# Optimization experiments

Hardware: AMD Instinct MI355X
Metric: run time of the kernel (lower is better)

Reference implementation:

```python
import jax, jax.numpy as jnp
import numpy as np

B, S, D, H, DFF = 4, 2048, 1024, 16, 4096
DK = D // H


def layer_norm(x, g, b, eps=1e-5):
    mu = jnp.mean(x, axis=-1, keepdims=True)
    var = jnp.mean((x - mu) ** 2, axis=-1, keepdims=True)
    return (x - mu) / jnp.sqrt(var + eps) * g + b


def setup_inputs() -> dict:
    key = jax.random.key(0)
    ks = jax.random.split(key, 16)
    w = lambda k, shape: jax.random.normal(k, shape, jnp.float32) * 0.02
    return {
        "x": jax.random.normal(ks[0], (B, S, D), jnp.float32),
        "w_q": w(ks[1], (D, D)), "b_q": jnp.zeros((D,), jnp.float32),
        "w_k": w(ks[2], (D, D)), "b_k": jnp.zeros((D,), jnp.float32),
        "w_v": w(ks[3], (D, D)), "b_v": jnp.zeros((D,), jnp.float32),
        "w_o": w(ks[4], (D, D)), "b_o": jnp.zeros((D,), jnp.float32),
        "w_g": w(ks[5], (D, H)), "b_g": jnp.zeros((H,), jnp.float32),
        "w1": w(ks[6], (D, DFF)), "b1": jnp.zeros((DFF,), jnp.float32),
        "w2": w(ks[7], (DFF, D)), "b2": jnp.zeros((D,), jnp.float32),
        "g1": jnp.ones((D,), jnp.float32), "beta1": jnp.zeros((D,), jnp.float32),
        "g2": jnp.ones((D,), jnp.float32), "beta2": jnp.zeros((D,), jnp.float32),
        "mask": jnp.ones((B, 1, 1, S), jnp.int32),
    }


def reference(x, w_q, b_q, w_k, b_k, w_v, b_v, w_o, b_o, w_g, b_g,
              w1, b1, w2, b2, g1, beta1, g2, beta2, mask):
    b, s, d = x.shape
    scale = DK ** -0.5
    # QKV projections -> [B,H,S,DK]
    q = (x @ w_q + b_q).reshape(b, s, H, DK).transpose(0, 2, 1, 3)
    k = (x @ w_k + b_k).reshape(b, s, H, DK).transpose(0, 2, 1, 3)
    v = (x @ w_v + b_v).reshape(b, s, H, DK).transpose(0, 2, 1, 3)
    scores = jnp.einsum("bhqd,bhkd->bhqk", q, k) * scale  # [B,H,S,S]
    scores = jnp.where(mask == 0, jnp.float32(-1e9), scores)
    attn = jax.nn.softmax(scores, axis=-1)
    # per-(token, head) sigmoid gate applied post-softmax
    gate = jax.nn.sigmoid(x @ w_g + b_g)            # [B,S,H]
    attn = attn * gate.transpose(0, 2, 1)[..., None]  # [B,H,S,1]
    ctx = jnp.einsum("bhqk,bhkd->bhqd", attn, v)
    ctx = ctx.transpose(0, 2, 1, 3).reshape(b, s, d)
    attn_out = ctx @ w_o + b_o
    x1 = layer_norm(x + attn_out, g1, beta1)
    ff = jax.nn.gelu(x1 @ w1 + b1, approximate=False) @ w2 + b2
    return layer_norm(x1 + ff, g2, beta2)
```

## Files before the change

### kernel.cpp

```cpp
#include <hip/hip_runtime.h>
#include <hip/hip_bf16.h>
#include <cstdint>


typedef __bf16 bf16x8 __attribute__((ext_vector_type(8)));
typedef float  f32x4  __attribute__((ext_vector_type(4)));

__device__ __forceinline__ uint16_t f2bf_bits(float f) {
    __hip_bfloat16 h = __float2bfloat16(f);
    return __builtin_bit_cast(uint16_t, h);
}

#define GLOAD16(ldsb, gp) __builtin_amdgcn_global_load_lds( \
    (const __attribute__((address_space(1))) void*)(gp),    \
    (__attribute__((address_space(3))) void*)(ldsb), 16, 0, 0)

__global__ __launch_bounds__(256) void cast_bf16_kernel(
    const float* __restrict__ in, __hip_bfloat16* __restrict__ out, size_t n4)
{
    size_t i = (size_t)blockIdx.x * blockDim.x + threadIdx.x;
    if (i >= n4) return;
    float4 v = ((const float4*)in)[i];
    ushort4 o;
    o.x = f2bf_bits(v.x); o.y = f2bf_bits(v.y);
    o.z = f2bf_bits(v.z); o.w = f2bf_bits(v.w);
    ((ushort4*)out)[i] = o;
}

__global__ __launch_bounds__(256) void transpose_cast_kernel(
    const float* __restrict__ in, __hip_bfloat16* __restrict__ out, int K, int N)
{
    __shared__ float t[32][33];
    int n0 = blockIdx.x * 32, k0 = blockIdx.y * 32;
    int tx = threadIdx.x, ty = threadIdx.y;
#pragma unroll
    for (int i = 0; i < 4; ++i)
        t[ty + i * 8][tx] = in[(size_t)(k0 + ty + i * 8) * N + n0 + tx];
    __syncthreads();
#pragma unroll
    for (int i = 0; i < 4; ++i)
        out[(size_t)(n0 + ty + i * 8) * K + k0 + tx] = __float2bfloat16(t[tx][ty + i * 8]);
}

__global__ __launch_bounds__(256) void gate_kernel(
    const float* __restrict__ x, const float* __restrict__ wg,
    const float* __restrict__ bg, float* __restrict__ gate)
{
    int tid = threadIdx.x, lane = tid & 63, wid = tid >> 6;
    int row = blockIdx.x * 4 + wid;
    const float* xr = x + (size_t)row * 1024;
    float acc[16];
#pragma unroll
    for (int hh = 0; hh < 16; ++hh) acc[hh] = 0.0f;
    for (int k = lane; k < 1024; k += 64) {
        float xv = xr[k];
        const float* wr = wg + (size_t)k * 16;
#pragma unroll
        for (int hh = 0; hh < 16; ++hh) acc[hh] = fmaf(xv, wr[hh], acc[hh]);
    }
#pragma unroll
    for (int hh = 0; hh < 16; ++hh) {
#pragma unroll
        for (int d = 1; d < 64; d <<= 1) acc[hh] += __shfl_xor(acc[hh], d);
    }
    if (lane < 16) {
        float v = 0.0f;
#pragma unroll
        for (int hh = 0; hh < 16; ++hh)
            if (lane == hh) v = acc[hh] + bg[hh];
        gate[(size_t)row * 16 + lane] = 1.0f / (1.0f + __expf(-v));
    }
}

__global__ __launch_bounds__(256) void ln_kernel(
    const float* __restrict__ A, const float* __restrict__ Bx,
    const float* __restrict__ g, const float* __restrict__ beta,
    float* __restrict__ outf, __hip_bfloat16* __restrict__ outb)
{
    int row = blockIdx.x, tid = threadIdx.x;
    const float4* a4 = (const float4*)(A  + (size_t)row * 1024);
    const float4* b4 = (const float4*)(Bx + (size_t)row * 1024);
    float4 va = a4[tid], vb = b4[tid];
    float x0 = va.x + vb.x, x1 = va.y + vb.y, x2 = va.z + vb.z, x3 = va.w + vb.w;
    float s  = x0 + x1 + x2 + x3;
    float sq = x0 * x0 + x1 * x1 + x2 * x2 + x3 * x3;
#pragma unroll
    for (int d = 1; d < 64; d <<= 1) { s += __shfl_xor(s, d); sq += __shfl_xor(sq, d); }
    __shared__ float ss[4], ssq[4];
    int wid = tid >> 6, lane = tid & 63;
    if (lane == 0) { ss[wid] = s; ssq[wid] = sq; }
    __syncthreads();
    s  = ss[0] + ss[1] + ss[2] + ss[3];
    sq = ssq[0] + ssq[1] + ssq[2] + ssq[3];
    float mean = s * (1.0f / 1024.0f);
    float var  = sq * (1.0f / 1024.0f) - mean * mean;
    float rstd = rsqrtf(var + 1e-5f);
    float4 gv = ((const float4*)g)[tid], bv = ((const float4*)beta)[tid];
    float y0 = (x0 - mean) * rstd * gv.x + bv.x;
    float y1 = (x1 - mean) * rstd * gv.y + bv.y;
    float y2 = (x2 - mean) * rstd * gv.z + bv.z;
    float y3 = (x3 - mean) * rstd * gv.w + bv.w;
    float4 o; o.x = y0; o.y = y1; o.z = y2; o.w = y3;
    ((float4*)(outf + (size_t)row * 1024))[tid] = o;
    if (outb) {
        ushort4 ob;
        ob.x = f2bf_bits(y0); ob.y = f2bf_bits(y1);
        ob.z = f2bf_bits(y2); ob.w = f2bf_bits(y3);
        ((ushort4*)(outb + (size_t)row * 1024))[tid] = ob;
    }
}

template<int EPI>
__global__ __launch_bounds__(256, 2) void gemm128(
    const __hip_bfloat16* __restrict__ A,
    const __hip_bfloat16* __restrict__ BT,
    const float* __restrict__ bias,
    void* __restrict__ Cout, int M, int N, int K)
{
    __shared__ __align__(16) __hip_bfloat16 As[128 * 64];
    __shared__ __align__(16) __hip_bfloat16 Bs[128 * 64];
    const int tid = threadIdx.x, lane = tid & 63, wid = tid >> 6;
    const int bx = blockIdx.x, by = blockIdx.y;
    const int wr = wid >> 1, wc = wid & 1;

    f32x4 acc[4][4];
#pragma unroll
    for (int i = 0; i < 4; ++i)
#pragma unroll
        for (int j = 0; j < 4; ++j) acc[i][j] = (f32x4){0.f, 0.f, 0.f, 0.f};

    const char* Abase = (const char*)A  + (size_t)(by * 128) * K * 2;
    const char* Bbase = (const char*)BT + (size_t)(bx * 128) * K * 2;
    char* AsB = (char*)As; char* BsB = (char*)Bs;
    const int laneRow = lane >> 3;
    const int laneCol = (lane & 7) * 16;

    for (int ks = 0; ks < K; ks += 64) {
#pragma unroll
        for (int j = 0; j < 4; ++j) {
            int r = j * 32 + wid * 8 + laneRow;
            size_t goff = (size_t)r * K * 2 + (size_t)ks * 2 + laneCol;
            GLOAD16(AsB + j * 4096 + wid * 1024, Abase + goff);
            GLOAD16(BsB + j * 4096 + wid * 1024, Bbase + goff);
        }
        __syncthreads();
#pragma unroll
        for (int kk = 0; kk < 2; ++kk) {
            const int kob = (kk * 32 + (lane >> 4) * 8) * 2;
            bf16x8 a[4], b[4];
#pragma unroll
            for (int mt = 0; mt < 4; ++mt)
                a[mt] = *(const bf16x8*)(AsB + (wr * 64 + mt * 16 + (lane & 15)) * 128 + kob);
#pragma unroll
            for (int nt = 0; nt < 4; ++nt)
                b[nt] = *(const bf16x8*)(BsB + (wc * 64 + nt * 16 + (lane & 15)) * 128 + kob);
#pragma unroll
            for (int mt = 0; mt < 4; ++mt)
#pragma unroll
                for (int nt = 0; nt < 4; ++nt)
                    acc[mt][nt] = __builtin_amdgcn_mfma_f32_16x16x32_bf16(
                        a[mt], b[nt], acc[mt][nt], 0, 0, 0);
        }
        __syncthreads();
    }

    const int m0 = by * 128 + wr * 64;
    const int n0 = bx * 128 + wc * 64;
#pragma unroll
    for (int mt = 0; mt < 4; ++mt) {
#pragma unroll
        for (int nt = 0; nt < 4; ++nt) {
            int n = n0 + nt * 16 + (lane & 15);
            float bv = bias[n];
#pragma unroll
            for (int j = 0; j < 4; ++j) {
                int m = m0 + mt * 16 + (lane >> 4) * 4 + j;
                float v = acc[mt][nt][j] + bv;
                ((float*)Cout)[(size_t)m * N + n] = v;
            }
        }
    }
}

template<int EPI>
__global__ __launch_bounds__(512, 2) void gemm256(
    const __hip_bfloat16* __restrict__ A,
    const __hip_bfloat16* __restrict__ BT,
    const float* __restrict__ bias0,
    const float* __restrict__ bias1,
    const float* __restrict__ bias2,
    __hip_bfloat16* __restrict__ out0,
    __hip_bfloat16* __restrict__ out1,
    __hip_bfloat16* __restrict__ out2,
    int M, int N, int K)
{
    __shared__ __align__(16) char lds_[131072];
    const int tid = threadIdx.x;
    const int lane = tid & 63;
    const int l15 = lane & 15;
    const int wid = tid >> 6;
    const int wm = wid >> 2, wn = wid & 3;

    const int NBX = N >> 8;
    const int cpx = ((M >> 8) * NBX) >> 3;
    const int nl = ((int)blockIdx.x & 7) * cpx + ((int)blockIdx.x >> 3);
    const int by = nl / NBX, bx = nl % NBX;

    const char* Abase = (const char*)A  + (size_t)(by * 256) * K * 2;
    const char* Bbase = (const char*)BT + (size_t)(bx * 256) * K * 2;

    const int srow = tid >> 3;
    const int ssw  = ((tid & 7) ^ (srow & 7)) * 16;

    f32x4 acc[8][4];
#pragma unroll
    for (int i = 0; i < 8; ++i)
#pragma unroll
        for (int j = 0; j < 4; ++j) acc[i][j] = (f32x4){0.f, 0.f, 0.f, 0.f};

    auto stageA = [&](int d, int c, int ks) {
        const char* src = Abase + ((size_t)(c * 64 + srow) * K + ks) * 2 + ssw;
        GLOAD16(lds_ + d * 65536 + c * 8192 + wid * 1024, src);
    };
    auto stageB = [&](int d, int c, int ks) {
        const char* src = Bbase + ((size_t)(c * 64 + srow) * K + ks) * 2 + ssw;
        GLOAD16(lds_ + d * 65536 + 32768 + c * 8192 + wid * 1024, src);
    };

    const int NT = K >> 6;
    stageB(0, 0, 0); stageB(0, 1, 0); stageB(0, 2, 0); stageB(0, 3, 0);
    stageA(0, 0, 0); stageA(0, 2, 0); stageA(0, 1, 0); stageA(0, 3, 0);
    asm volatile("s_waitcnt vmcnt(0)" ::: "memory");
    __builtin_amdgcn_s_barrier();

    for (int t = 0; t < NT; ++t) {
        const int cur = t & 1, nxt = cur ^ 1;
        const int ksn = (t + 1) << 6;
        const bool st = (t + 1 < NT);
        const char* ldsA = lds_ + cur * 65536;
        const char* ldsB = ldsA + 32768;

        bf16x8 bfr[4][2];
#pragma unroll
        for (int p = 0; p < 4; ++p) {
            if (p == 0) {
#pragma unroll
                for (int nf = 0; nf < 4; ++nf) {
                    const int br = wn * 64 + nf * 16 + l15;
#pragma unroll
                    for (int kk = 0; kk < 2; ++kk) {
                        const int kb = kk * 64 + (lane >> 4) * 16;
                        bfr[nf][kk] = *(const bf16x8*)(ldsB + (br >> 6) * 8192 +
                            (br & 63) * 128 + (kb ^ ((br & 7) << 4)));
                    }
                }
            }
            bf16x8 afr[2][2];
#pragma unroll
            for (int mi = 0; mi < 2; ++mi) {
                const int ar = wm * 128 + (2 * p + mi) * 16 + l15;
#pragma unroll
                for (int kk = 0; kk < 2; ++kk) {
                    const int kb = kk * 64 + (lane >> 4) * 16;
                    afr[mi][kk] = *(const bf16x8*)(ldsA + (ar >> 6) * 8192 +
                        (ar & 63) * 128 + (kb ^ ((ar & 7) << 4)));
                }
            }
            if (st) {
                if      (p == 0) { stageB(nxt, 0, ksn); stageB(nxt, 1, ksn); }
                else if (p == 1) { stageB(nxt, 2, ksn); stageB(nxt, 3, ksn); }
                else if (p == 2) { stageA(nxt, 0, ksn); stageA(nxt, 2, ksn); }
                else             { stageA(nxt, 1, ksn); stageA(nxt, 3, ksn); }
            }
            __builtin_amdgcn_s_barrier();
            __builtin_amdgcn_s_setprio(1);
#pragma unroll
            for (int mi = 0; mi < 2; ++mi)
#pragma unroll
                for (int nf = 0; nf < 4; ++nf)
#pragma unroll
                    for (int kk = 0; kk < 2; ++kk)
                        acc[2 * p + mi][nf] = __builtin_amdgcn_mfma_f32_16x16x32_bf16(
                            afr[mi][kk], bfr[nf][kk], acc[2 * p + mi][nf], 0, 0, 0);
            __builtin_amdgcn_s_setprio(0);
            if (p == 1) asm volatile("s_waitcnt vmcnt(4)" ::: "memory");
            if (p == 3) asm volatile("s_waitcnt vmcnt(2)" ::: "memory");
            __builtin_amdgcn_s_barrier();
        }
    }

    const int nbase = bx * 256 + wn * 64;
    const int mbase = by * 256 + wm * 128;
    if constexpr (EPI == 5) {
        const int reg = nbase >> 10;
        const float* bias = (reg == 0) ? bias0 : (reg == 1) ? bias1 : bias2;
#pragma unroll
        for (int mf = 0; mf < 8; ++mf) {
#pragma unroll
            for (int nf = 0; nf < 4; ++nf) {
                const int n = nbase + nf * 16 + l15;
                const int nn = n & 1023, h = nn >> 6, dk = nn & 63;
                const float bv = bias[nn];
#pragma unroll
                for (int j = 0; j < 4; ++j) {
                    const int m = mbase + mf * 16 + (lane >> 4) * 4 + j;
                    const int b = m >> 11, s = m & 2047;
                    const float v = acc[mf][nf][j] + bv;
                    if (reg == 0)
                        out0[((((size_t)b * 16 + h) * 2048 + s) << 6) + dk] =
                            __float2bfloat16(v * 0.125f);
                    else if (reg == 1)
                        out1[((((size_t)b * 16 + h) * 2048 + s) << 6) + dk] =
                            __float2bfloat16(v);
                    else
                        out2[(((size_t)b * 16 + h) * 64 + dk) * 2048 + s] =
                            __float2bfloat16(v);
                }
            }
        }
    } else {
#pragma unroll
        for (int mf = 0; mf < 8; ++mf) {
#pragma unroll
            for (int nf = 0; nf < 4; ++nf) {
                const int n = nbase + nf * 16 + l15;
                const float bv = bias0[n];
#pragma unroll
                for (int j = 0; j < 4; ++j) {
                    const int m = mbase + mf * 16 + (lane >> 4) * 4 + j;
                    const float v = acc[mf][nf][j] + bv;
                    const float ge = 0.5f * v * (1.0f + erff(v * 0.70710678118654752f));
                    out0[(size_t)m * N + n] = __float2bfloat16(ge);
                }
            }
        }
    }
}

__global__ __launch_bounds__(256, 2) void attn_kernel(
    const __hip_bfloat16* __restrict__ Q,
    const __hip_bfloat16* __restrict__ Kg,
    const __hip_bfloat16* __restrict__ Vt,
    const float* __restrict__ gate,
    const int* __restrict__ mask,
    __hip_bfloat16* __restrict__ ctx)
{
    __shared__ __align__(16) __hip_bfloat16 Ks[64 * 64];
    __shared__ __align__(16) __hip_bfloat16 Vs[64 * 64];
    __shared__ __align__(16) __hip_bfloat16 Ps[4][16 * 64];
    const int tid = threadIdx.x, lane = tid & 63, wid = tid >> 6;

    int lin = blockIdx.x;
    int nl  = (lin & 7) * 256 + (lin >> 3);
    const int bh = nl >> 5, qt = nl & 31;
    const int b = bh >> 4, h = bh & 15;
    const int q0 = qt * 64 + wid * 16;

    bf16x8 aq[2];
    const __hip_bfloat16* Qbase = Q + ((size_t)bh * 2048 + q0) * 64;
#pragma unroll
    for (int kk = 0; kk < 2; ++kk)
        aq[kk] = *(const bf16x8*)(Qbase + (lane & 15) * 64 + kk * 32 + (lane >> 4) * 8);

    f32x4 octx[4];
#pragma unroll
    for (int dt = 0; dt < 4; ++dt) octx[dt] = (f32x4){0.f, 0.f, 0.f, 0.f};
    float l_part[4] = {0.f, 0.f, 0.f, 0.f};
    float m_cur = 0.0f;

    const char* Kbase = (const char*)(Kg + (size_t)bh * 2048 * 64);
    const char* Vbase = (const char*)(Vt + (size_t)bh * 64 * 2048);
    char* KsB = (char*)Ks; char* VsB = (char*)Vs;
    char* PsB = (char*)&Ps[wid][0];

    const int srow = (lane >> 3);
    const int schunk = lane & 7;

    for (int kv0 = 0; kv0 < 2048; kv0 += 64) {
#pragma unroll
        for (int j = 0; j < 2; ++j) {
            int off = j * 4096 + wid * 1024;
            int row = j * 32 + wid * 8 + srow;
            int sc  = (schunk ^ (row & 7)) * 16;
            GLOAD16(KsB + off, Kbase + (size_t)(kv0 + row) * 128 + sc);
            GLOAD16(VsB + off, Vbase + (size_t)row * 4096 + (size_t)kv0 * 2 + sc);
        }
        float madd[4];
#pragma unroll
        for (int ct = 0; ct < 4; ++ct) {
            int kvi = kv0 + ct * 16 + (lane & 15);
            madd[ct] = (mask[b * 2048 + kvi] == 0) ? -1e9f : 0.0f;
        }
        __syncthreads();

        f32x4 sfr[4];
#pragma unroll
        for (int ct = 0; ct < 4; ++ct) sfr[ct] = (f32x4){0.f, 0.f, 0.f, 0.f};
        __builtin_amdgcn_s_setprio(1);
#pragma unroll
        for (int kk = 0; kk < 2; ++kk) {
            const int kob = (kk * 32 + (lane >> 4) * 8) * 2;
#pragma unroll
            for (int ct = 0; ct < 4; ++ct) {
                int krow = ct * 16 + (lane & 15);
                bf16x8 bk = *(const bf16x8*)(KsB + ((krow * 128 + kob) ^ ((krow & 7) << 4)));
                sfr[ct] = __builtin_amdgcn_mfma_f32_16x16x32_bf16(aq[kk], bk, sfr[ct], 0, 0, 0);
            }
        }
        __builtin_amdgcn_s_setprio(0);
#pragma unroll
        for (int ct = 0; ct < 4; ++ct) {
#pragma unroll
            for (int r = 0; r < 4; ++r) sfr[ct][r] += madd[ct];
        }

        float mlane = sfr[0][0];
#pragma unroll
        for (int ct = 0; ct < 4; ++ct)
#pragma unroll
            for (int r = 0; r < 4; ++r) mlane = fmaxf(mlane, sfr[ct][r]);

        if (kv0 == 0) {
            float wm = mlane;
#pragma unroll
            for (int d = 1; d < 64; d <<= 1) wm = fmaxf(wm, __shfl_xor(wm, d));
            m_cur = wm;
        } else if (!__all(mlane <= m_cur + 8.0f)) {
            float wm = mlane;
#pragma unroll
            for (int d = 1; d < 64; d <<= 1) wm = fmaxf(wm, __shfl_xor(wm, d));
            wm = fmaxf(wm, m_cur);
            float c = __expf(m_cur - wm);
            m_cur = wm;
#pragma unroll
            for (int dt = 0; dt < 4; ++dt)
#pragma unroll
                for (int r = 0; r < 4; ++r) octx[dt][r] *= c;
#pragma unroll
            for (int r = 0; r < 4; ++r) l_part[r] *= c;
        }

#pragma unroll
        for (int ct = 0; ct < 4; ++ct) {
#pragma unroll
            for (int r = 0; r < 4; ++r) {
                float p = __expf(sfr[ct][r] - m_cur);
                l_part[r] += p;
                int qr = (lane >> 4) * 4 + r;
                int byteoff = (qr * 128 + (ct * 16 + (lane & 15)) * 2) ^ ((qr & 7) << 4);
                *(__hip_bfloat16*)(PsB + byteoff) = __float2bfloat16(p);
            }
        }
        __builtin_amdgcn_s_setprio(1);
#pragma unroll
        for (int kk = 0; kk < 2; ++kk) {
            const int kb = kk * 32 + (lane >> 4) * 8;
            int pbyte = ((lane & 15) * 128 + kb * 2) ^ (((lane & 15) & 7) << 4);
            bf16x8 ap = *(const bf16x8*)(PsB + pbyte);
#pragma unroll
            for (int dt = 0; dt < 4; ++dt) {
                int vrow = dt * 16 + (lane & 15);
                bf16x8 bvv = *(const bf16x8*)(VsB + ((vrow * 128 + kb * 2) ^ ((vrow & 7) << 4)));
                octx[dt] = __builtin_amdgcn_mfma_f32_16x16x32_bf16(ap, bvv, octx[dt], 0, 0, 0);
            }
        }
        __builtin_amdgcn_s_setprio(0);
        __syncthreads();
    }

#pragma unroll
    for (int r = 0; r < 4; ++r) {
        float s = l_part[r];
        s += __shfl_xor(s, 1); s += __shfl_xor(s, 2);
        s += __shfl_xor(s, 4); s += __shfl_xor(s, 8);
        l_part[r] = s;
    }

#pragma unroll
    for (int r = 0; r < 4; ++r) {
        int qg = q0 + (lane >> 4) * 4 + r;
        size_t rowm = (size_t)b * 2048 + qg;
        float gv = gate[rowm * 16 + h];
        float inv = gv / l_part[r];
#pragma unroll
        for (int dt = 0; dt < 4; ++dt)
            ctx[rowm * 1024 + h * 64 + dt * 16 + (lane & 15)] =
                __float2bfloat16(octx[dt][r] * inv);
    }
}

extern "C" void kernel_launch(void* const* d_in, const int* in_sizes, int n_in,
                              void* d_out, int out_size, void* d_ws, size_t ws_size,
                              hipStream_t stream)
{
    const float* x    = (const float*)d_in[0];
    const float* w_q  = (const float*)d_in[1];
    const float* b_q  = (const float*)d_in[2];
    const float* w_k  = (const float*)d_in[3];
    const float* b_k  = (const float*)d_in[4];
    const float* w_v  = (const float*)d_in[5];
    const float* b_v  = (const float*)d_in[6];
    const float* w_o  = (const float*)d_in[7];
    const float* b_o  = (const float*)d_in[8];
    const float* w_g  = (const float*)d_in[9];
    const float* b_g  = (const float*)d_in[10];
    const float* w1   = (const float*)d_in[11];
    const float* b1   = (const float*)d_in[12];
    const float* w2   = (const float*)d_in[13];
    const float* b2   = (const float*)d_in[14];
    const float* g1   = (const float*)d_in[15];
    const float* be1  = (const float*)d_in[16];
    const float* g2   = (const float*)d_in[17];
    const float* be2  = (const float*)d_in[18];
    const int*   mask = (const int*)d_in[19];

    char* ws = (char*)d_ws;
    size_t off = 0;
    auto alloc = [&](size_t bytes) -> char* {
        char* p = ws + off; off += (bytes + 255) & ~(size_t)255; return p;
    };

    char* regionA = alloc(67108864);
    __hip_bfloat16* xb   = (__hip_bfloat16*)regionA;
    __hip_bfloat16* qb   = (__hip_bfloat16*)(regionA + 16777216);
    __hip_bfloat16* kb   = (__hip_bfloat16*)(regionA + 33554432);
    __hip_bfloat16* vb   = (__hip_bfloat16*)(regionA + 50331648);
    __hip_bfloat16* hbuf = (__hip_bfloat16*)regionA;

    __hip_bfloat16* wqT = (__hip_bfloat16*)alloc(2097152);
    __hip_bfloat16* wkT = (__hip_bfloat16*)alloc(2097152);
    __hip_bfloat16* wvT = (__hip_bfloat16*)alloc(2097152);
    __hip_bfloat16* woT = (__hip_bfloat16*)alloc(2097152);
    __hip_bfloat16* w1T = (__hip_bfloat16*)alloc(8388608);
    __hip_bfloat16* w2T = (__hip_bfloat16*)alloc(8388608);
    float* gate       = (float*)alloc(524288);
    __hip_bfloat16* ctx = (__hip_bfloat16*)alloc(16777216);
    float* attn_out   = (float*)alloc(33554432);
    float* x1f        = (float*)alloc(33554432);
    __hip_bfloat16* x1b = (__hip_bfloat16*)alloc(16777216);

    dim3 tb(32, 8);
    cast_bf16_kernel<<<8192, 256, 0, stream>>>(x, xb, 2097152);
    transpose_cast_kernel<<<dim3(32, 32),  tb, 0, stream>>>(w_q, wqT, 1024, 1024);
    transpose_cast_kernel<<<dim3(32, 32),  tb, 0, stream>>>(w_k, wkT, 1024, 1024);
    transpose_cast_kernel<<<dim3(32, 32),  tb, 0, stream>>>(w_v, wvT, 1024, 1024);
    transpose_cast_kernel<<<dim3(32, 32),  tb, 0, stream>>>(w_o, woT, 1024, 1024);
    transpose_cast_kernel<<<dim3(128, 32), tb, 0, stream>>>(w1, w1T, 1024, 4096);
    transpose_cast_kernel<<<dim3(32, 128), tb, 0, stream>>>(w2, w2T, 4096, 1024);
    gate_kernel<<<2048, 256, 0, stream>>>(x, w_g, b_g, gate);

    gemm256<5><<<384, 512, 0, stream>>>(xb, wqT, b_q, b_k, b_v, qb, kb, vb,
                                        8192, 3072, 1024);

    attn_kernel<<<2048, 256, 0, stream>>>(qb, kb, vb, gate, mask, ctx);

    gemm128<0><<<dim3(8, 64), 256, 0, stream>>>(ctx, woT, b_o, attn_out, 8192, 1024, 1024);
    ln_kernel<<<8192, 256, 0, stream>>>(x, attn_out, g1, be1, x1f, x1b);
    gemm256<6><<<512, 512, 0, stream>>>(x1b, w1T, b1, nullptr, nullptr,
                                        hbuf, nullptr, nullptr, 8192, 4096, 1024);
    gemm128<0><<<dim3(8, 64), 256, 0, stream>>>(hbuf, w2T, b2, attn_out, 8192, 1024, 4096);
    ln_kernel<<<8192, 256, 0, stream>>>(x1f, attn_out, g2, be2, (float*)d_out, nullptr);
}
```

Measured before the change: 666.9 us.

## Split fused QKV GEMM into three gemm128 launches; use exp2 softmax with log2e-folded Q scale

Replaces the single fused 256-tile QKV projection with three separate 128-tile GEMM launches, each writing its own head-major layout through new epilogue variants. The Q epilogue now folds log2(e) into the 1/sqrt(dk) scale so attention can use exp2f instead of __expf. The lazy-rescale threshold is raised to match the base-2 units. This trades the larger, more efficient fused GEMM for three smaller launches that reread the activations, so the projection step may lose efficiency while the softmax exponentials get cheaper.

```diff
diff --git a/kernel.cpp b/kernel.cpp
--- a/kernel.cpp
+++ b/kernel.cpp
@@ -14,6 +14,8 @@
 #define GLOAD16(ldsb, gp) __builtin_amdgcn_global_load_lds( \
     (const __attribute__((address_space(1))) void*)(gp),    \
     (__attribute__((address_space(3))) void*)(ldsb), 16, 0, 0)
+
+#define QSCALE_LOG2E 0.18033688011112f
 
 __global__ __launch_bounds__(256) void cast_bf16_kernel(
     const float* __restrict__ in, __hip_bfloat16* __restrict__ out, size_t n4)
@@ -176,7 +178,21 @@
             for (int j = 0; j < 4; ++j) {
                 int m = m0 + mt * 16 + (lane >> 4) * 4 + j;
                 float v = acc[mt][nt][j] + bv;
-                ((float*)Cout)[(size_t)m * N + n] = v;
+                if constexpr (EPI == 0) {
+                    ((float*)Cout)[(size_t)m * N + n] = v;
+                } else if constexpr (EPI == 1) {
+                    int b = m >> 11, s = m & 2047, h = n >> 6, dk = n & 63;
+                    ((__hip_bfloat16*)Cout)[((((size_t)b * 16 + h) * 2048 + s) << 6) + dk] =
+                        __float2bfloat16(v * QSCALE_LOG2E);
+                } else if constexpr (EPI == 2) {
+                    int b = m >> 11, s = m & 2047, h = n >> 6, dk = n & 63;
+                    ((__hip_bfloat16*)Cout)[((((size_t)b * 16 + h) * 2048 + s) << 6) + dk] =
+                        __float2bfloat16(v);
+                } else if constexpr (EPI == 3) {
+                    int b = m >> 11, s = m & 2047, h = n >> 6, dk = n & 63;
+                    ((__hip_bfloat16*)Cout)[(((size_t)b * 16 + h) * 64 + dk) * 2048 + s] =
+                        __float2bfloat16(v);
+                }
             }
         }
     }
@@ -187,11 +203,7 @@
     const __hip_bfloat16* __restrict__ A,
     const __hip_bfloat16* __restrict__ BT,
     const float* __restrict__ bias0,
-    const float* __restrict__ bias1,
-    const float* __restrict__ bias2,
     __hip_bfloat16* __restrict__ out0,
-    __hip_bfloat16* __restrict__ out1,
-    __hip_bfloat16* __restrict__ out2,
     int M, int N, int K)
 {
     __shared__ __align__(16) char lds_[131072];
@@ -291,47 +303,18 @@
 
     const int nbase = bx * 256 + wn * 64;
     const int mbase = by * 256 + wm * 128;
-    if constexpr (EPI == 5) {
-        const int reg = nbase >> 10;
-        const float* bias = (reg == 0) ? bias0 : (reg == 1) ? bias1 : bias2;
-#pragma unroll
-        for (int mf = 0; mf < 8; ++mf) {
-#pragma unroll
-            for (int nf = 0; nf < 4; ++nf) {
-                const int n = nbase + nf * 16 + l15;
-                const int nn = n & 1023, h = nn >> 6, dk = nn & 63;
-                const float bv = bias[nn];
-#pragma unroll
-                for (int j = 0; j < 4; ++j) {
-                    const int m = mbase + mf * 16 + (lane >> 4) * 4 + j;
-                    const int b = m >> 11, s = m & 2047;
-                    const float v = acc[mf][nf][j] + bv;
-                    if (reg == 0)
-                        out0[((((size_t)b * 16 + h) * 2048 + s) << 6) + dk] =
-                            __float2bfloat16(v * 0.125f);
-                    else if (reg == 1)
-                        out1[((((size_t)b * 16 + h) * 2048 + s) << 6) + dk] =
-                            __float2bfloat16(v);
-                    else
-                        out2[(((size_t)b * 16 + h) * 64 + dk) * 2048 + s] =
-                            __float2bfloat16(v);
-                }
-            }
-        }
-    } else {
-#pragma unroll
-        for (int mf = 0; mf < 8; ++mf) {
-#pragma unroll
-            for (int nf = 0; nf < 4; ++nf) {
-                const int n = nbase + nf * 16 + l15;
-                const float bv = bias0[n];
-#pragma unroll
-                for (int j = 0; j < 4; ++j) {
-                    const int m = mbase + mf * 16 + (lane >> 4) * 4 + j;
-                    const float v = acc[mf][nf][j] + bv;
-                    const float ge = 0.5f * v * (1.0f + erff(v * 0.70710678118654752f));
-                    out0[(size_t)m * N + n] = __float2bfloat16(ge);
-                }
+#pragma unroll
+    for (int mf = 0; mf < 8; ++mf) {
+#pragma unroll
+        for (int nf = 0; nf < 4; ++nf) {
+            const int n = nbase + nf * 16 + l15;
+            const float bv = bias0[n];
+#pragma unroll
+            for (int j = 0; j < 4; ++j) {
+                const int m = mbase + mf * 16 + (lane >> 4) * 4 + j;
+                const float v = acc[mf][nf][j] + bv;
+                const float ge = 0.5f * v * (1.0f + erff(v * 0.70710678118654752f));
+                out0[(size_t)m * N + n] = __float2bfloat16(ge);
             }
         }
     }
@@ -425,12 +408,12 @@
 #pragma unroll
             for (int d = 1; d < 64; d <<= 1) wm = fmaxf(wm, __shfl_xor(wm, d));
             m_cur = wm;
-        } else if (!__all(mlane <= m_cur + 8.0f)) {
+        } else if (!__all(mlane <= m_cur + 11.0f)) {
             float wm = mlane;
 #pragma unroll
             for (int d = 1; d < 64; d <<= 1) wm = fmaxf(wm, __shfl_xor(wm, d));
             wm = fmaxf(wm, m_cur);
-            float c = __expf(m_cur - wm);
+            float c = exp2f(m_cur - wm);
             m_cur = wm;
 #pragma unroll
             for (int dt = 0; dt < 4; ++dt)
@@ -444,7 +427,7 @@
         for (int ct = 0; ct < 4; ++ct) {
 #pragma unroll
             for (int r = 0; r < 4; ++r) {
-                float p = __expf(sfr[ct][r] - m_cur);
+                float p = exp2f(sfr[ct][r] - m_cur);
                 l_part[r] += p;
                 int qr = (lane >> 4) * 4 + r;
                 int byteoff = (qr * 128 + (ct * 16 + (lane & 15)) * 2) ^ ((qr & 7) << 4);
@@ -549,15 +532,16 @@
     transpose_cast_kernel<<<dim3(32, 128), tb, 0, stream>>>(w2, w2T, 4096, 1024);
     gate_kernel<<<2048, 256, 0, stream>>>(x, w_g, b_g, gate);
 
-    gemm256<5><<<384, 512, 0, stream>>>(xb, wqT, b_q, b_k, b_v, qb, kb, vb,
-                                        8192, 3072, 1024);
+    dim3 g1024(8, 64);
+    gemm128<1><<<g1024, 256, 0, stream>>>(xb, wqT, b_q, qb, 8192, 1024, 1024);
+    gemm128<2><<<g1024, 256, 0, stream>>>(xb, wkT, b_k, kb, 8192, 1024, 1024);
+    gemm128<3><<<g1024, 256, 0, stream>>>(xb, wvT, b_v, vb, 8192, 1024, 1024);
 
     attn_kernel<<<2048, 256, 0, stream>>>(qb, kb, vb, gate, mask, ctx);
 
-    gemm128<0><<<dim3(8, 64), 256, 0, stream>>>(ctx, woT, b_o, attn_out, 8192, 1024, 1024);
+    gemm128<0><<<g1024, 256, 0, stream>>>(ctx, woT, b_o, attn_out, 8192, 1024, 1024);
     ln_kernel<<<8192, 256, 0, stream>>>(x, attn_out, g1, be1, x1f, x1b);
-    gemm256<6><<<512, 512, 0, stream>>>(x1b, w1T, b1, nullptr, nullptr,
-                                        hbuf, nullptr, nullptr, 8192, 4096, 1024);
-    gemm128<0><<<dim3(8, 64), 256, 0, stream>>>(hbuf, w2T, b2, attn_out, 8192, 1024, 4096);
+    gemm256<6><<<512, 512, 0, stream>>>(x1b, w1T, b1, hbuf, 8192, 4096, 1024);
+    gemm128<0><<<g1024, 256, 0, stream>>>(hbuf, w2T, b2, attn_out, 8192, 1024, 4096);
     ln_kernel<<<8192, 256, 0, stream>>>(x1f, attn_out, g2, be2, (float*)d_out, nullptr);
 }
```

New measurement: 687.5 us. 1.03x slower.
